# Kernel optimization log

Hardware: AMD Instinct MI355X
Metric: run time of the kernel (lower is better)

## Reference

```python
import jax, jax.numpy as jnp
import numpy as np
import math

D_MODEL = 1024
NUM_HEADS = 16
GROUPS = 4
HPG = NUM_HEADS // GROUPS  # heads per group
DK = D_MODEL // NUM_HEADS


def setup_inputs() -> dict:
    key = jax.random.key(0)
    ks = jax.random.split(key, 11)
    B, S = 1, 4096
    scale = 1.0 / math.sqrt(D_MODEL)
    inp = {
        "q": jax.random.normal(ks[0], (B, S, D_MODEL), jnp.float32),
        "k": jax.random.normal(ks[1], (B, S, D_MODEL), jnp.float32),
        "v": jax.random.normal(ks[2], (B, S, D_MODEL), jnp.float32),
        # nn.Linear weights stored [out, in], applied as x @ W.T + b
        "Wq": jax.random.normal(ks[3], (D_MODEL, D_MODEL), jnp.float32) * scale,
        "bq": jax.random.normal(ks[4], (D_MODEL,), jnp.float32) * scale,
        "Wk": jax.random.normal(ks[5], (D_MODEL, D_MODEL), jnp.float32) * scale,
        "bk": jax.random.normal(ks[6], (D_MODEL,), jnp.float32) * scale,
        "Wv": jax.random.normal(ks[7], (D_MODEL, D_MODEL), jnp.float32) * scale,
        "bv": jax.random.normal(ks[8], (D_MODEL,), jnp.float32) * scale,
        "Wo": jax.random.normal(ks[9], (D_MODEL, D_MODEL), jnp.float32) * scale,
        "bo": jax.random.normal(ks[10], (D_MODEL,), jnp.float32) * scale,
    }
    return inp


def _reshape_qkv(x):
    # [b, s, d_model] -> [b, groups, hpg, s, dk]
    b, s, _ = x.shape
    x = x.reshape(b, s, GROUPS, HPG, DK)
    return x.transpose(0, 2, 3, 1, 4)


def reference(q, k, v, Wq, bq, Wk, bk, Wv, bv, Wo, bo):
    b, s, _ = q.shape
    query = _reshape_qkv(q @ Wq.T + bq)  # [b,g,h,s,dk]
    key_ = _reshape_qkv(k @ Wk.T + bk)
    value = _reshape_qkv(v @ Wv.T + bv)

    scores = jnp.einsum('bghqd,bghkd->bghqk', query, key_) / math.sqrt(DK)
    causal = jnp.tril(jnp.ones((s, s), dtype=bool))  # [s_q, s_k]
    scores = jnp.where(causal, scores, -jnp.inf)
    attn = jax.nn.softmax(scores, axis=-1)

    out = jnp.einsum('bghqk,bghkd->bghqd', attn, value)
    out = out.transpose(0, 3, 1, 2, 4).reshape(b, s, NUM_HEADS * DK)
    return out @ Wo.T + bo, key_, value
```

## Files before the change

### kernel.cpp

```cpp
#include <hip/hip_runtime.h>
#include <math.h>

typedef __attribute__((ext_vector_type(8))) __bf16 bf16x8;
typedef __attribute__((ext_vector_type(8))) unsigned short ushort8;
typedef __attribute__((ext_vector_type(4))) float f32x4;
typedef unsigned short ushort_t;
typedef unsigned int uint_t;

#define MFMA16(a,b,c) __builtin_amdgcn_mfma_f32_16x16x32_bf16(a,b,c,0,0,0)

#define GLD16(gp, lp) __builtin_amdgcn_global_load_lds( \
  (__attribute__((address_space(1))) const void*)(gp), \
  (__attribute__((address_space(3))) void*)(lp), 16, 0, 0)

__device__ __forceinline__ ushort_t f2bf(float f) {
  uint_t u = __builtin_bit_cast(uint_t, f);
  u = (u + 0x7fffu + ((u >> 16) & 1u)) >> 16;
  return (ushort_t)u;
}

struct ConvArgs {
  const float* src[7];
  ushort_t* dst[7];
  int cum[8];
};

__global__ __launch_bounds__(256) void convall(ConvArgs a) {
  int flat = blockIdx.x * 256 + threadIdx.x;
  int s = 0;
#pragma unroll
  for (int i = 1; i < 7; ++i) if (flat >= a.cum[i]) s = i;
  int idx = flat - a.cum[s];
  float4 v = ((const float4*)a.src[s])[idx];
  ushort4 o;
  o.x = f2bf(v.x); o.y = f2bf(v.y); o.z = f2bf(v.z); o.w = f2bf(v.w);
  ((ushort4*)a.dst[s])[idx] = o;
}

struct QKVArgs {
  const ushort_t* A[3];
  const ushort_t* B[3];
  const float* bias[3];
  float* outf[3];
  ushort_t* outb[3];
};

__global__ __launch_bounds__(256)
void qkv_gemm(QKVArgs ar) {
  const int M = 4096, K = 1024;
  const int z = blockIdx.z;
  const ushort_t* __restrict__ A = ar.A[z];
  const ushort_t* __restrict__ B = ar.B[z];
  const float* __restrict__ bias = ar.bias[z];

  __shared__ __align__(16) ushort_t Al[128 * 32];
  __shared__ __align__(16) ushort_t Bl[128 * 32];
  const int tid = threadIdx.x;
  const int w = tid >> 6, l = tid & 63;
  const int lr = l & 15, lg = l >> 4;
  const int bm = blockIdx.x * 128, bn = blockIdx.y * 128;
  const int wr = w >> 1, wc = w & 1;
  f32x4 acc[4][4] = {};

  const int crow = l >> 2;
  const int ccol = (l & 3) * 8;

  for (int k0 = 0; k0 < K; k0 += 32) {
    __syncthreads();
#pragma unroll
    for (int i = 0; i < 2; ++i) {
      const int c = w * 2 + i;
      GLD16(A + (size_t)(bm + c * 16 + crow) * K + k0 + ccol, &Al[c * 512]);
      GLD16(B + (size_t)(bn + c * 16 + crow) * K + k0 + ccol, &Bl[c * 512]);
    }
    __syncthreads();
    bf16x8 af[4], bfr[4];
#pragma unroll
    for (int mi = 0; mi < 4; ++mi)
      af[mi] = *(const bf16x8*)&Al[(wr * 64 + mi * 16 + lr) * 32 + lg * 8];
#pragma unroll
    for (int ni = 0; ni < 4; ++ni)
      bfr[ni] = *(const bf16x8*)&Bl[(wc * 64 + ni * 16 + lr) * 32 + lg * 8];
#pragma unroll
    for (int mi = 0; mi < 4; ++mi)
#pragma unroll
      for (int ni = 0; ni < 4; ++ni)
        acc[mi][ni] = MFMA16(af[mi], bfr[ni], acc[mi][ni]);
  }

  float* outf = ar.outf[z];
  ushort_t* outb = ar.outb[z];
#pragma unroll
  for (int mi = 0; mi < 4; ++mi) {
#pragma unroll
    for (int ni = 0; ni < 4; ++ni) {
      const int r0 = bm + wr * 64 + mi * 16 + lg * 4;
      const int cc = bn + wc * 64 + ni * 16 + lr;
      const float bv = bias[cc];
      const int hh = cc >> 6, dk = cc & 63;
      const int dh = dk >> 5, lgk = (dk & 31) >> 3, jq = dk & 7;
#pragma unroll
      for (int jj = 0; jj < 4; ++jj) {
        float v = acc[mi][ni][jj] + bv;
        int s = r0 + jj;
        if (z == 0) {
          size_t idx = ((((size_t)hh * 256 + (s >> 4)) * 2 + dh) * 64 + (s & 15) + 16 * lgk) * 8 + jq;
          outb[idx] = f2bf(v * 0.18033688011112042f);
        } else if (z == 1) {
          outf[((size_t)hh * M + s) * 64 + dk] = v;
          size_t idx = ((((size_t)hh * 256 + (s >> 4)) * 2 + dh) * 64 + (s & 15) + 16 * lgk) * 8 + jq;
          outb[idx] = f2bf(v);
        } else {
          outf[((size_t)hh * M + s) * 64 + dk] = v;
        }
      }
    }
  }
}

__global__ __launch_bounds__(256)
void gemm_o(const ushort_t* __restrict__ A, const ushort_t* __restrict__ B,
            const float* __restrict__ bias, float* __restrict__ Cout)
{
  const int N = 1024, K = 1024;
  __shared__ __align__(16) ushort_t Al[128 * 32];
  __shared__ __align__(16) ushort_t Bl[128 * 32];
  const int tid = threadIdx.x;
  const int w = tid >> 6, l = tid & 63;
  const int lr = l & 15, lg = l >> 4;
  const int bm = blockIdx.x * 128, bn = blockIdx.y * 128;
  const int wr = w >> 1, wc = w & 1;
  f32x4 acc[4][4] = {};
  const int crow = l >> 2;
  const int ccol = (l & 3) * 8;

  for (int k0 = 0; k0 < K; k0 += 32) {
    __syncthreads();
#pragma unroll
    for (int i = 0; i < 2; ++i) {
      const int c = w * 2 + i;
      GLD16(A + (size_t)(bm + c * 16 + crow) * K + k0 + ccol, &Al[c * 512]);
      GLD16(B + (size_t)(bn + c * 16 + crow) * K + k0 + ccol, &Bl[c * 512]);
    }
    __syncthreads();
    bf16x8 af[4], bfr[4];
#pragma unroll
    for (int mi = 0; mi < 4; ++mi)
      af[mi] = *(const bf16x8*)&Al[(wr * 64 + mi * 16 + lr) * 32 + lg * 8];
#pragma unroll
    for (int ni = 0; ni < 4; ++ni)
      bfr[ni] = *(const bf16x8*)&Bl[(wc * 64 + ni * 16 + lr) * 32 + lg * 8];
#pragma unroll
    for (int mi = 0; mi < 4; ++mi)
#pragma unroll
      for (int ni = 0; ni < 4; ++ni)
        acc[mi][ni] = MFMA16(af[mi], bfr[ni], acc[mi][ni]);
  }

#pragma unroll
  for (int mi = 0; mi < 4; ++mi)
#pragma unroll
    for (int ni = 0; ni < 4; ++ni) {
      const int r0 = bm + wr * 64 + mi * 16 + lg * 4;
      const int cc = bn + wc * 64 + ni * 16 + lr;
      const float bv = bias[cc];
#pragma unroll
      for (int jj = 0; jj < 4; ++jj)
        Cout[(size_t)(r0 + jj) * N + cc] = acc[mi][ni][jj] + bv;
    }
}

__global__ __launch_bounds__(256) void pack_vt(const float* __restrict__ Vhead,
                                               ushort_t* __restrict__ Vt) {
  const int S = 4096;
  int tile = blockIdx.x * 4 + (threadIdx.x >> 6);
  int l = threadIdx.x & 63;
  int h = tile >> 9, rem = tile & 511;
  int kb = rem >> 2, dvt = rem & 3;
  int lr = l & 15, lg = l >> 4;
  const float* src = Vhead + ((size_t)h * S + kb * 32 + lg * 8) * 64 + dvt * 16 + lr;
  ushort8 o8;
#pragma unroll
  for (int j = 0; j < 8; ++j) o8[j] = f2bf(src[(size_t)j * 64]);
  *(ushort8*)&Vt[(size_t)tile * 512 + l * 8] = o8;
}

__global__ __launch_bounds__(256, 2)
void attn(const ushort_t* __restrict__ Qt, const ushort_t* __restrict__ Kt,
          const ushort_t* __restrict__ Vt, ushort_t* __restrict__ Ao) {
  const int DM = 1024;
  const int h = blockIdx.y;
  const int T = 31 - (int)blockIdx.x;
  const int tid = threadIdx.x, w = tid >> 6, l = tid & 63;
  const int lr = l & 15, lg = l >> 4;
  const int qw = T * 128 + w * 32;

  __shared__ __align__(16) ushort_t plds[4][32 * 64];
  char* pw = (char*)plds[w];
  const uint_t swz = (uint_t)(lr & 7) << 4;

  const size_t hQ = (size_t)h * 256;

  bf16x8 qf[2][2];
#pragma unroll
  for (int qt = 0; qt < 2; ++qt)
#pragma unroll
    for (int dh = 0; dh < 2; ++dh)
      qf[qt][dh] = *(const bf16x8*)&Qt[(((hQ + (qw >> 4) + qt) * 2 + dh) << 9) + l * 8];

  f32x4 o[2][4] = {};
  float m[2], lsum[2];
#pragma unroll
  for (int qt = 0; qt < 2; ++qt) { m[qt] = -__builtin_inff(); lsum[qt] = 0.0f; }

  bf16x8 kc[8], kn[8], vf[8];

  auto loadK8 = [&](bf16x8* dst, int kt) {
#pragma unroll
    for (int kt4 = 0; kt4 < 4; ++kt4)
#pragma unroll
      for (int dh = 0; dh < 2; ++dh)
        dst[kt4 * 2 + dh] =
            *(const bf16x8*)&Kt[(((hQ + (kt >> 4) + kt4) * 2 + dh) << 9) + l * 8];
  };
  auto loadV8 = [&](int kt) {
#pragma unroll
    for (int ks = 0; ks < 2; ++ks)
#pragma unroll
      for (int dvt = 0; dvt < 4; ++dvt)
        vf[ks * 4 + dvt] =
            *(const bf16x8*)&Vt[((((size_t)h * 128 + (kt >> 5) + ks) * 4 + dvt) << 9) + l * 8];
  };

  auto step = [&](int kt, bool domask, bool pf) {
    loadV8(kt);
    if (pf) loadK8(kn, kt + 64);
    f32x4 st[4][2];
#pragma unroll
    for (int kt4 = 0; kt4 < 4; ++kt4) {
      f32x4 c0 = {}, c1 = {};
      c0 = MFMA16(kc[kt4 * 2 + 0], qf[0][0], c0);
      c0 = MFMA16(kc[kt4 * 2 + 1], qf[0][1], c0);
      c1 = MFMA16(kc[kt4 * 2 + 0], qf[1][0], c1);
      c1 = MFMA16(kc[kt4 * 2 + 1], qf[1][1], c1);
      st[kt4][0] = c0;
      st[kt4][1] = c1;
    }
    if (domask) {
#pragma unroll
      for (int kt4 = 0; kt4 < 4; ++kt4)
#pragma unroll
        for (int qt = 0; qt < 2; ++qt) {
          int qq = qw + qt * 16 + lr;
#pragma unroll
          for (int jj = 0; jj < 4; ++jj) {
            int key = kt + kt4 * 16 + lg * 4 + jj;
            if (key > qq) st[kt4][qt][jj] = -__builtin_inff();
          }
        }
    }
#pragma unroll
    for (int qt = 0; qt < 2; ++qt) {
      float pm = -__builtin_inff();
#pragma unroll
      for (int kt4 = 0; kt4 < 4; ++kt4)
#pragma unroll
        for (int jj = 0; jj < 4; ++jj)
          pm = fmaxf(pm, st[kt4][qt][jj]);
      pm = fmaxf(pm, __shfl_xor(pm, 16));
      pm = fmaxf(pm, __shfl_xor(pm, 32));
      float mn = fmaxf(m[qt], pm);
      float al = __builtin_amdgcn_exp2f(m[qt] - mn);
      m[qt] = mn;
      float ps = 0.0f;
#pragma unroll
      for (int kt4 = 0; kt4 < 4; ++kt4) {
#pragma unroll
        for (int jj = 0; jj < 4; ++jj) {
          float e = __builtin_amdgcn_exp2f(st[kt4][qt][jj] - mn);
          st[kt4][qt][jj] = e;
          ps += e;
        }
      }
      ps += __shfl_xor(ps, 16);
      ps += __shfl_xor(ps, 32);
      lsum[qt] = lsum[qt] * al + ps;
#pragma unroll
      for (int dvt = 0; dvt < 4; ++dvt) {
#pragma unroll
        for (int jj = 0; jj < 4; ++jj) o[qt][dvt][jj] *= al;
      }
#pragma unroll
      for (int kt4 = 0; kt4 < 4; ++kt4) {
        ushort4 pk;
        pk.x = f2bf(st[kt4][qt][0]); pk.y = f2bf(st[kt4][qt][1]);
        pk.z = f2bf(st[kt4][qt][2]); pk.w = f2bf(st[kt4][qt][3]);
        uint_t bo = (uint_t)(qt * 16 + lr) * 128 + (uint_t)(kt4 * 32 + lg * 8);
        *(ushort4*)(pw + (bo ^ swz)) = pk;
      }
    }
    bf16x8 pa[2][2];
#pragma unroll
    for (int qt = 0; qt < 2; ++qt)
#pragma unroll
      for (int ks = 0; ks < 2; ++ks) {
        uint_t bo = (uint_t)(qt * 16 + lr) * 128 + (uint_t)(ks * 64 + lg * 16);
        pa[qt][ks] = *(const bf16x8*)(pw + (bo ^ swz));
      }
#pragma unroll
    for (int dvt = 0; dvt < 4; ++dvt)
#pragma unroll
      for (int ks = 0; ks < 2; ++ks) {
        o[0][dvt] = MFMA16(vf[ks * 4 + dvt], pa[0][ks], o[0][dvt]);
        o[1][dvt] = MFMA16(vf[ks * 4 + dvt], pa[1][ks], o[1][dvt]);
      }
    if (pf) {
#pragma unroll
      for (int i = 0; i < 8; ++i) kc[i] = kn[i];
    }
  };

  const int ktm = qw & ~63;
  loadK8(kc, 0);
  for (int kt = 0; kt < ktm; kt += 64) step(kt, false, true);
  step(ktm, true, false);

#pragma unroll
  for (int qt = 0; qt < 2; ++qt) {
    float inv = 1.0f / lsum[qt];
#pragma unroll
    for (int dvt = 0; dvt < 4; ++dvt) {
      ushort4 pk;
      pk.x = f2bf(o[qt][dvt][0] * inv);
      pk.y = f2bf(o[qt][dvt][1] * inv);
      pk.z = f2bf(o[qt][dvt][2] * inv);
      pk.w = f2bf(o[qt][dvt][3] * inv);
      *(ushort4*)&Ao[(size_t)(qw + qt * 16 + lr) * DM + h * 64 + dvt * 16 + lg * 4] = pk;
    }
  }
}

extern "C" void kernel_launch(void* const* d_in, const int* in_sizes, int n_in,
                              void* d_out, int out_size, void* d_ws, size_t ws_size,
                              hipStream_t stream) {
  const int S = 4096, DM = 1024;
  const size_t NE = (size_t)S * DM;

  const float* q  = (const float*)d_in[0];
  const float* k  = (const float*)d_in[1];
  const float* v  = (const float*)d_in[2];
  const float* Wq = (const float*)d_in[3];
  const float* bq = (const float*)d_in[4];
  const float* Wk = (const float*)d_in[5];
  const float* bk = (const float*)d_in[6];
  const float* Wv = (const float*)d_in[7];
  const float* bv = (const float*)d_in[8];
  const float* Wo = (const float*)d_in[9];
  const float* bo = (const float*)d_in[10];

  unsigned char* ws = (unsigned char*)d_ws;
  ushort_t* qb  = (ushort_t*)(ws);
  ushort_t* kb  = (ushort_t*)(ws + (8u << 20));
  ushort_t* vb  = (ushort_t*)(ws + (16u << 20));
  ushort_t* wqb = (ushort_t*)(ws + (24u << 20));
  ushort_t* wkb = (ushort_t*)(ws + (26u << 20));
  ushort_t* wvb = (ushort_t*)(ws + (28u << 20));
  ushort_t* wob = (ushort_t*)(ws + (30u << 20));
  ushort_t* qpb = (ushort_t*)(ws + (32u << 20));
  ushort_t* kpb = (ushort_t*)(ws + (40u << 20));
  ushort_t* vt  = kb;
  ushort_t* ao  = qb;

  float* outO = (float*)d_out;
  float* keyO = outO + NE;
  float* valO = keyO + NE;

  ConvArgs ca;
  ca.src[0] = q;  ca.src[1] = k;  ca.src[2] = v;
  ca.src[3] = Wq; ca.src[4] = Wk; ca.src[5] = Wv; ca.src[6] = Wo;
  ca.dst[0] = qb;  ca.dst[1] = kb;  ca.dst[2] = vb;
  ca.dst[3] = wqb; ca.dst[4] = wkb; ca.dst[5] = wvb; ca.dst[6] = wob;
  const int NB = 1048576, WB = 262144;
  ca.cum[0] = 0;
  ca.cum[1] = NB; ca.cum[2] = 2 * NB; ca.cum[3] = 3 * NB;
  ca.cum[4] = 3 * NB + WB; ca.cum[5] = 3 * NB + 2 * WB;
  ca.cum[6] = 3 * NB + 3 * WB; ca.cum[7] = 3 * NB + 4 * WB;
  convall<<<ca.cum[7] / 256, 256, 0, stream>>>(ca);

  QKVArgs qa;
  qa.A[0] = qb;  qa.A[1] = kb;  qa.A[2] = vb;
  qa.B[0] = wqb; qa.B[1] = wkb; qa.B[2] = wvb;
  qa.bias[0] = bq; qa.bias[1] = bk; qa.bias[2] = bv;
  qa.outf[0] = nullptr; qa.outf[1] = keyO; qa.outf[2] = valO;
  qa.outb[0] = qpb;     qa.outb[1] = kpb;  qa.outb[2] = nullptr;
  qkv_gemm<<<dim3(S / 128, DM / 128, 3), 256, 0, stream>>>(qa);

  pack_vt<<<2048, 256, 0, stream>>>(valO, vt);

  attn<<<dim3(S / 128, 16), 256, 0, stream>>>(qpb, kpb, vt, ao);

  gemm_o<<<dim3(S / 128, DM / 128), 256, 0, stream>>>(ao, wob, bo, outO);
}
```

Before: 315.3 us.

## Rebalance causal attention with paired 16-row tiles, XCD-aware head mapping, lazy rescale

The attention kernel now gives each wave one 16-query tile instead of 32 rows and pairs tile t with tile 255-t, so every wave does about the same amount of causal work. The grid becomes flat and maps heads by XCD index so blocks of the same head share an L2. It also skips the online-softmax rescale unless the running max grows by more than a threshold, and uses the hardware bf16 convert. Each K/V fragment load now feeds half as many MFMAs, which may raise memory traffic, and the lazy rescale costs a little numerical headroom.

```diff
diff --git a/kernel.cpp b/kernel.cpp
--- a/kernel.cpp
+++ b/kernel.cpp
@@ -17,6 +17,10 @@
   uint_t u = __builtin_bit_cast(uint_t, f);
   u = (u + 0x7fffu + ((u >> 16) & 1u)) >> 16;
   return (ushort_t)u;
+}
+__device__ __forceinline__ ushort_t f2bfn(float f) {
+  __bf16 b = (__bf16)f;
+  return __builtin_bit_cast(ushort_t, b);
 }
 
 struct ConvArgs {
@@ -185,157 +189,142 @@
   *(ushort8*)&Vt[(size_t)tile * 512 + l * 8] = o8;
 }
 
-__global__ __launch_bounds__(256, 2)
+__global__ __launch_bounds__(256)
 void attn(const ushort_t* __restrict__ Qt, const ushort_t* __restrict__ Kt,
           const ushort_t* __restrict__ Vt, ushort_t* __restrict__ Ao) {
   const int DM = 1024;
-  const int h = blockIdx.y;
-  const int T = 31 - (int)blockIdx.x;
+  const int flat = blockIdx.x;
+  const int xcd = flat & 7, i = flat >> 3;
+  const int h = xcd * 2 + (i & 1);
+  const int b = i >> 1;
   const int tid = threadIdx.x, w = tid >> 6, l = tid & 63;
   const int lr = l & 15, lg = l >> 4;
-  const int qw = T * 128 + w * 32;
-
-  __shared__ __align__(16) ushort_t plds[4][32 * 64];
+  const int t_lo = b * 4 + w;
+
+  __shared__ __align__(16) ushort_t plds[4][1024];
   char* pw = (char*)plds[w];
   const uint_t swz = (uint_t)(lr & 7) << 4;
 
   const size_t hQ = (size_t)h * 256;
-
-  bf16x8 qf[2][2];
-#pragma unroll
-  for (int qt = 0; qt < 2; ++qt)
+  const ushort_t* __restrict__ Vh = Vt + (size_t)h * 262144;
+
+#pragma unroll 1
+  for (int seg = 0; seg < 2; ++seg) {
+    const int t = seg ? (255 - t_lo) : t_lo;
+    const int qw = t * 16;
+
+    bf16x8 qf[2];
 #pragma unroll
     for (int dh = 0; dh < 2; ++dh)
-      qf[qt][dh] = *(const bf16x8*)&Qt[(((hQ + (qw >> 4) + qt) * 2 + dh) << 9) + l * 8];
-
-  f32x4 o[2][4] = {};
-  float m[2], lsum[2];
-#pragma unroll
-  for (int qt = 0; qt < 2; ++qt) { m[qt] = -__builtin_inff(); lsum[qt] = 0.0f; }
-
-  bf16x8 kc[8], kn[8], vf[8];
-
-  auto loadK8 = [&](bf16x8* dst, int kt) {
-#pragma unroll
-    for (int kt4 = 0; kt4 < 4; ++kt4)
-#pragma unroll
-      for (int dh = 0; dh < 2; ++dh)
-        dst[kt4 * 2 + dh] =
-            *(const bf16x8*)&Kt[(((hQ + (kt >> 4) + kt4) * 2 + dh) << 9) + l * 8];
-  };
-  auto loadV8 = [&](int kt) {
-#pragma unroll
-    for (int ks = 0; ks < 2; ++ks)
-#pragma unroll
-      for (int dvt = 0; dvt < 4; ++dvt)
-        vf[ks * 4 + dvt] =
-            *(const bf16x8*)&Vt[((((size_t)h * 128 + (kt >> 5) + ks) * 4 + dvt) << 9) + l * 8];
-  };
-
-  auto step = [&](int kt, bool domask, bool pf) {
-    loadV8(kt);
-    if (pf) loadK8(kn, kt + 64);
-    f32x4 st[4][2];
-#pragma unroll
-    for (int kt4 = 0; kt4 < 4; ++kt4) {
-      f32x4 c0 = {}, c1 = {};
-      c0 = MFMA16(kc[kt4 * 2 + 0], qf[0][0], c0);
-      c0 = MFMA16(kc[kt4 * 2 + 1], qf[0][1], c0);
-      c1 = MFMA16(kc[kt4 * 2 + 0], qf[1][0], c1);
-      c1 = MFMA16(kc[kt4 * 2 + 1], qf[1][1], c1);
-      st[kt4][0] = c0;
-      st[kt4][1] = c1;
-    }
-    if (domask) {
+      qf[dh] = *(const bf16x8*)&Qt[(((hQ + t) * 2 + dh) << 9) + l * 8];
+
+    f32x4 o[4] = {};
+    float m = -__builtin_inff(), lsum = 0.0f;
+
+    bf16x8 kc[8], kn[8], vf[8];
+    auto loadK8 = [&](bf16x8* dst, int kt) {
 #pragma unroll
       for (int kt4 = 0; kt4 < 4; ++kt4)
 #pragma unroll
-        for (int qt = 0; qt < 2; ++qt) {
-          int qq = qw + qt * 16 + lr;
+        for (int dh = 0; dh < 2; ++dh)
+          dst[kt4 * 2 + dh] =
+              *(const bf16x8*)&Kt[(((hQ + (kt >> 4) + kt4) * 2 + dh) << 9) + l * 8];
+    };
+
+    const int ktm = qw & ~63;
+    loadK8(kc, 0);
+    for (int kt = 0; kt <= ktm; kt += 64) {
+#pragma unroll
+      for (int ks = 0; ks < 2; ++ks)
+#pragma unroll
+        for (int dvt = 0; dvt < 4; ++dvt)
+          vf[ks * 4 + dvt] =
+              *(const bf16x8*)&Vh[(((size_t)(kt >> 5) + ks) * 4 + dvt) << 9 | (l * 8)];
+      const bool last = (kt == ktm);
+      if (!last) loadK8(kn, kt + 64);
+
+      f32x4 st[4];
+#pragma unroll
+      for (int kt4 = 0; kt4 < 4; ++kt4) {
+        f32x4 c = {};
+        c = MFMA16(kc[kt4 * 2 + 0], qf[0], c);
+        c = MFMA16(kc[kt4 * 2 + 1], qf[1], c);
+        st[kt4] = c;
+      }
+      if (last) {
+        int qq = qw + lr;
+#pragma unroll
+        for (int kt4 = 0; kt4 < 4; ++kt4)
 #pragma unroll
           for (int jj = 0; jj < 4; ++jj) {
             int key = kt + kt4 * 16 + lg * 4 + jj;
-            if (key > qq) st[kt4][qt][jj] = -__builtin_inff();
+            if (key > qq) st[kt4][jj] = -__builtin_inff();
           }
-        }
-    }
-#pragma unroll
-    for (int qt = 0; qt < 2; ++qt) {
-      float pm = -__builtin_inff();
-#pragma unroll
-      for (int kt4 = 0; kt4 < 4; ++kt4)
-#pragma unroll
-        for (int jj = 0; jj < 4; ++jj)
-          pm = fmaxf(pm, st[kt4][qt][jj]);
+      }
+      float a0 = fmaxf(fmaxf(st[0][0], st[0][1]), fmaxf(st[0][2], st[0][3]));
+      float a1 = fmaxf(fmaxf(st[1][0], st[1][1]), fmaxf(st[1][2], st[1][3]));
+      float a2 = fmaxf(fmaxf(st[2][0], st[2][1]), fmaxf(st[2][2], st[2][3]));
+      float a3 = fmaxf(fmaxf(st[3][0], st[3][1]), fmaxf(st[3][2], st[3][3]));
+      float pm = fmaxf(fmaxf(a0, a1), fmaxf(a2, a3));
       pm = fmaxf(pm, __shfl_xor(pm, 16));
       pm = fmaxf(pm, __shfl_xor(pm, 32));
-      float mn = fmaxf(m[qt], pm);
-      float al = __builtin_amdgcn_exp2f(m[qt] - mn);
-      m[qt] = mn;
+      if (__any(pm > m + 10.0f)) {
+        float mn = fmaxf(m, pm);
+        float al = __builtin_amdgcn_exp2f(m - mn);
+        m = mn;
+        lsum *= al;
+#pragma unroll
+        for (int dvt = 0; dvt < 4; ++dvt)
+#pragma unroll
+          for (int jj = 0; jj < 4; ++jj) o[dvt][jj] *= al;
+      }
       float ps = 0.0f;
 #pragma unroll
-      for (int kt4 = 0; kt4 < 4; ++kt4) {
+      for (int kt4 = 0; kt4 < 4; ++kt4)
 #pragma unroll
         for (int jj = 0; jj < 4; ++jj) {
-          float e = __builtin_amdgcn_exp2f(st[kt4][qt][jj] - mn);
-          st[kt4][qt][jj] = e;
+          float e = __builtin_amdgcn_exp2f(st[kt4][jj] - m);
+          st[kt4][jj] = e;
           ps += e;
         }
-      }
       ps += __shfl_xor(ps, 16);
       ps += __shfl_xor(ps, 32);
-      lsum[qt] = lsum[qt] * al + ps;
-#pragma unroll
-      for (int dvt = 0; dvt < 4; ++dvt) {
-#pragma unroll
-        for (int jj = 0; jj < 4; ++jj) o[qt][dvt][jj] *= al;
-      }
+      lsum += ps;
 #pragma unroll
       for (int kt4 = 0; kt4 < 4; ++kt4) {
         ushort4 pk;
-        pk.x = f2bf(st[kt4][qt][0]); pk.y = f2bf(st[kt4][qt][1]);
-        pk.z = f2bf(st[kt4][qt][2]); pk.w = f2bf(st[kt4][qt][3]);
-        uint_t bo = (uint_t)(qt * 16 + lr) * 128 + (uint_t)(kt4 * 32 + lg * 8);
+        pk.x = f2bfn(st[kt4][0]); pk.y = f2bfn(st[kt4][1]);
+        pk.z = f2bfn(st[kt4][2]); pk.w = f2bfn(st[kt4][3]);
+        uint_t bo = (uint_t)lr * 128 + (uint_t)(kt4 * 32 + lg * 8);
         *(ushort4*)(pw + (bo ^ swz)) = pk;
       }
-    }
-    bf16x8 pa[2][2];
-#pragma unroll
-    for (int qt = 0; qt < 2; ++qt)
+      bf16x8 pa[2];
 #pragma unroll
       for (int ks = 0; ks < 2; ++ks) {
-        uint_t bo = (uint_t)(qt * 16 + lr) * 128 + (uint_t)(ks * 64 + lg * 16);
-        pa[qt][ks] = *(const bf16x8*)(pw + (bo ^ swz));
-      }
-#pragma unroll
-    for (int dvt = 0; dvt < 4; ++dvt)
-#pragma unroll
-      for (int ks = 0; ks < 2; ++ks) {
-        o[0][dvt] = MFMA16(vf[ks * 4 + dvt], pa[0][ks], o[0][dvt]);
-        o[1][dvt] = MFMA16(vf[ks * 4 + dvt], pa[1][ks], o[1][dvt]);
-      }
-    if (pf) {
-#pragma unroll
-      for (int i = 0; i < 8; ++i) kc[i] = kn[i];
-    }
-  };
-
-  const int ktm = qw & ~63;
-  loadK8(kc, 0);
-  for (int kt = 0; kt < ktm; kt += 64) step(kt, false, true);
-  step(ktm, true, false);
-
-#pragma unroll
-  for (int qt = 0; qt < 2; ++qt) {
-    float inv = 1.0f / lsum[qt];
+        uint_t bo = (uint_t)lr * 128 + (uint_t)(ks * 64 + lg * 16);
+        pa[ks] = *(const bf16x8*)(pw + (bo ^ swz));
+      }
+#pragma unroll
+      for (int dvt = 0; dvt < 4; ++dvt)
+#pragma unroll
+        for (int ks = 0; ks < 2; ++ks)
+          o[dvt] = MFMA16(vf[ks * 4 + dvt], pa[ks], o[dvt]);
+
+      if (!last) {
+#pragma unroll
+        for (int r = 0; r < 8; ++r) kc[r] = kn[r];
+      }
+    }
+
+    float inv = 1.0f / lsum;
 #pragma unroll
     for (int dvt = 0; dvt < 4; ++dvt) {
       ushort4 pk;
-      pk.x = f2bf(o[qt][dvt][0] * inv);
-      pk.y = f2bf(o[qt][dvt][1] * inv);
-      pk.z = f2bf(o[qt][dvt][2] * inv);
-      pk.w = f2bf(o[qt][dvt][3] * inv);
-      *(ushort4*)&Ao[(size_t)(qw + qt * 16 + lr) * DM + h * 64 + dvt * 16 + lg * 4] = pk;
+      pk.x = f2bfn(o[dvt][0] * inv);
+      pk.y = f2bfn(o[dvt][1] * inv);
+      pk.z = f2bfn(o[dvt][2] * inv);
+      pk.w = f2bfn(o[dvt][3] * inv);
+      *(ushort4*)&Ao[(size_t)(qw + lr) * DM + h * 64 + dvt * 16 + lg * 4] = pk;
     }
   }
 }
@@ -397,7 +386,7 @@
 
   pack_vt<<<2048, 256, 0, stream>>>(valO, vt);
 
-  attn<<<dim3(S / 128, 16), 256, 0, stream>>>(qpb, kpb, vt, ao);
+  attn<<<512, 256, 0, stream>>>(qpb, kpb, vt, ao);
 
   gemm_o<<<dim3(S / 128, DM / 128), 256, 0, stream>>>(ao, wob, bo, outO);
 }
```

New measurement: 266.7 us. 1.18x faster.
